# Kernel optimization log

Measured on AMD Instinct MI355X. Metric: run time of the kernel, lower is better.

Reference implementation:

```python
import jax, jax.numpy as jnp
import numpy as np

B, S, H = 1, 2048, 4096
NH = 32
HD = H // NH  # 128
HALF = HD // 2
BASE = 10000.0


def setup_inputs() -> dict:
    key = jax.random.key(0)
    k1, k2, k3 = jax.random.split(key, 3)
    hidden_states = jax.random.normal(k1, (B, S, H), dtype=jnp.float32)
    W_qkv = jax.random.normal(k2, (H, 3 * H), dtype=jnp.float32) * 0.02
    W_o = jax.random.normal(k3, (H, H), dtype=jnp.float32) * 0.02
    # causal additive mask [B,1,S,S]: 0 on/below diagonal, large negative above
    causal = jnp.triu(jnp.full((S, S), -1e9, dtype=jnp.float32), k=1)
    attention_mask = jnp.broadcast_to(causal[None, None], (B, 1, S, S))
    position_ids = jnp.broadcast_to(jnp.arange(S, dtype=jnp.int64)[None, :], (B, S))
    return {
        'hidden_states': hidden_states,
        'W_qkv': W_qkv,
        'W_o': W_o,
        'attention_mask': attention_mask,
        'position_ids': position_ids,
    }


def _rope(x, cos, sin):
    # x: [b,s,nh,hd]; cos/sin: [b,s,1,half]. Half-split rotation as in the Triton kernel.
    x1, x2 = x[..., :HALF], x[..., HALF:]
    return jnp.concatenate([x1 * cos - x2 * sin, x1 * sin + x2 * cos], axis=-1)


def reference(hidden_states, W_qkv, W_o, attention_mask, position_ids):
    b, s, h = hidden_states.shape
    # fused QKV projection (dequantized GPTQ matmul == dense matmul math)
    qkv = jnp.einsum('bsh,hk->bsk', hidden_states, W_qkv).reshape(b, s, 3, NH, HD)
    # RoPE angles: freq = exp(col * INV_BASE) * position_id, INV_BASE = -2 ln(base)/head_dim
    inv_base = -2.0 * np.log(BASE) / HD
    freqs = jnp.exp(jnp.arange(HALF, dtype=jnp.float32) * inv_base)  # [half]
    theta = position_ids.astype(jnp.float32)[:, :, None] * freqs      # [b,s,half]
    cos = jnp.cos(theta)[:, :, None, :]
    sin = jnp.sin(theta)[:, :, None, :]
    q = _rope(qkv[:, :, 0], cos, sin).transpose(0, 2, 1, 3)  # [b,nh,s,hd]
    k = _rope(qkv[:, :, 1], cos, sin).transpose(0, 2, 1, 3)
    v = qkv[:, :, 2].transpose(0, 2, 1, 3)
    scores = jnp.einsum('bhqd,bhkd->bhqk', q, k) / np.sqrt(HD).astype(np.float32)
    scores = scores + attention_mask
    scores = jnp.maximum(scores, jnp.finfo(scores.dtype).min)
    attn = jax.nn.softmax(scores.astype(jnp.float32), axis=-1).astype(q.dtype)
    out = jnp.einsum('bhqk,bhkd->bqhd', attn, v).reshape(b, s, h)
    return jnp.einsum('bsh,ho->bso', out, W_o)
```

## Files before the change

kernel.cpp:

```cpp
#include <hip/hip_runtime.h>

#define S_LEN 2048
#define HDIM 4096
#define NHEADS 32
#define HEAD_DIM 128
#define HALF_DIM 64
#define N_QKV 12288
#define QK_COLS 8192

typedef __attribute__((ext_vector_type(8))) short short8;
typedef __attribute__((ext_vector_type(4))) float f32x4;

typedef const __attribute__((address_space(1))) unsigned int gu32;
typedef __attribute__((address_space(3))) unsigned int lu32;

__device__ __forceinline__ void gload_lds16(const void* g, void* l) {
    __builtin_amdgcn_global_load_lds((gu32*)g, (lu32*)l, 16, 0, 0);
}

__device__ __forceinline__ unsigned short f2bf(float f) {
    unsigned int u = __float_as_uint(f);
    u += 0x7fff + ((u >> 16) & 1);
    return (unsigned short)(u >> 16);
}

__device__ __forceinline__ void xcd_map(int& bx, int& by) {
    int gx = gridDim.x;
    int lin = blockIdx.y * gx + blockIdx.x;
    int x = lin & 7, c = lin >> 3;
    int bxp = gx >> 3;
    bx = bxp * x + c % bxp;
    by = c / bxp;
}


__global__ __launch_bounds__(256) void cvt_hs_k(const float* __restrict__ in,
                                                unsigned short* __restrict__ out, int n4) {
    int i = blockIdx.x * 256 + threadIdx.x;
    if (i >= n4) return;
    float4 v = reinterpret_cast<const float4*>(in)[i];
    ushort4 o;
    o.x = f2bf(v.x); o.y = f2bf(v.y); o.z = f2bf(v.z); o.w = f2bf(v.w);
    reinterpret_cast<ushort4*>(out)[i] = o;
}

__device__ __forceinline__ int permute_col(int n) {
    if (n < QK_COLS) {
        int hd = n & 127;
        int base = n - hd;
        int e = hd & 63;
        int d2 = (e & 15) + 32 * (e >> 4) + ((hd >> 6) << 4);
        return base + d2;
    }
    return n;
}

template <bool PERM>
__global__ __launch_bounds__(256) void tconv_k(const float* __restrict__ in,
                                               unsigned short* __restrict__ out, int R, int C) {
    __shared__ float tile[64][65];
    int c0 = blockIdx.x * 64, r0 = blockIdx.y * 64;
    int tx = threadIdx.x & 63, ty = threadIdx.x >> 6;
#pragma unroll
    for (int i = 0; i < 16; ++i) {
        int r = ty + i * 4;
        tile[r][tx] = in[(size_t)(r0 + r) * C + c0 + tx];
    }
    __syncthreads();
#pragma unroll
    for (int i = 0; i < 16; ++i) {
        int c = ty + i * 4;
        int n = PERM ? permute_col(c0 + c) : (c0 + c);
        out[(size_t)n * R + r0 + tx] = f2bf(tile[tx][c]);
    }
}

__global__ __launch_bounds__(256) void rope_tab_k(const int* __restrict__ pos_raw,
                                                  float* __restrict__ ctab,
                                                  float* __restrict__ stab) {
    int i = blockIdx.x * 256 + threadIdx.x;
    int s = i >> 6, d = i & 63;
    bool is64 = (pos_raw[1] == 0 && pos_raw[2] == 1);
    int p = is64 ? pos_raw[2 * s] : pos_raw[s];
    const float INVB = -0.14391156831212787f;
    float freq = expf((float)d * INVB);
    float th = (float)p * freq;
    ctab[i] = cosf(th);
    stab[i] = sinf(th);
}


__device__ __forceinline__ void mainloop(const unsigned short* __restrict__ Ag,
                                         const unsigned short* __restrict__ Bg,
                                         int K, int m0, int n0,
                                         char* As, char* Bs,
                                         f32x4 (&acc)[4][4]) {
    const int tid = threadIdx.x;
    const int wid = tid >> 6, lane = tid & 63, l15 = lane & 15, l4 = lane >> 4;
    const int wm = wid >> 1, wn = wid & 1;
    const int NT = K >> 6;

    size_t abase[4], bbase[4];
    int off[4];
#pragma unroll
    for (int i = 0; i < 4; ++i) {
        int p = (i * 256 + tid) << 4;
        int q = p ^ (((p >> 7) & 7) << 4);
        abase[i] = (size_t)(m0 + (q >> 7)) * K + ((q & 127) >> 1);
        bbase[i] = (size_t)(n0 + (q >> 7)) * K + ((q & 127) >> 1);
        off[i] = p;
    }

    for (int t = 0; t < NT; ++t) {
        int k0 = t << 6;
#pragma unroll
        for (int i = 0; i < 4; ++i) gload_lds16(Ag + abase[i] + k0, As + off[i]);
#pragma unroll
        for (int i = 0; i < 4; ++i) gload_lds16(Bg + bbase[i] + k0, Bs + off[i]);
        asm volatile("s_waitcnt vmcnt(0)" ::: "memory");
        __builtin_amdgcn_s_barrier();

        short8 a[4][2], b[4][2];
#pragma unroll
        for (int am = 0; am < 4; ++am)
#pragma unroll
            for (int ks = 0; ks < 2; ++ks) {
                int lin = ((wm * 64 + am * 16 + l15) << 7) + ks * 64 + l4 * 16;
                a[am][ks] = *(const short8*)(As + (lin ^ (((lin >> 7) & 7) << 4)));
            }
#pragma unroll
        for (int bn = 0; bn < 4; ++bn)
#pragma unroll
            for (int ks = 0; ks < 2; ++ks) {
                int lin = ((wn * 64 + bn * 16 + l15) << 7) + ks * 64 + l4 * 16;
                b[bn][ks] = *(const short8*)(Bs + (lin ^ (((lin >> 7) & 7) << 4)));
            }
#pragma unroll
        for (int ks = 0; ks < 2; ++ks)
#pragma unroll
            for (int am = 0; am < 4; ++am)
#pragma unroll
                for (int bn = 0; bn < 4; ++bn)
                    acc[am][bn] = __builtin_amdgcn_mfma_f32_16x16x32_bf16(a[am][ks], b[bn][ks], acc[am][bn], 0, 0, 0);

        __builtin_amdgcn_s_barrier();
    }
}

__global__ __launch_bounds__(256, 3) void gemm1_k(const unsigned short* __restrict__ A,
                                                  const unsigned short* __restrict__ Bt,
                                                  const float* __restrict__ ctab,
                                                  const float* __restrict__ stab,
                                                  unsigned short* __restrict__ qb,
                                                  unsigned short* __restrict__ kb,
                                                  unsigned short* __restrict__ vt) {
    __shared__ __attribute__((aligned(16))) char As[16384];
    __shared__ __attribute__((aligned(16))) char Bs[16384];

    int bx, by;
    xcd_map(bx, by);
    int m0 = by * 128, n0 = bx * 128;

    f32x4 acc[4][4];
#pragma unroll
    for (int i = 0; i < 4; ++i)
#pragma unroll
        for (int j = 0; j < 4; ++j) acc[i][j] = (f32x4){0.f, 0.f, 0.f, 0.f};

    mainloop(A, Bt, HDIM, m0, n0, As, Bs, acc);

    int tid = threadIdx.x, wid = tid >> 6, lane = tid & 63, l15 = lane & 15, l4 = lane >> 4;
    int wm = wid >> 1, wn = wid & 1;
    int which = n0 >> 12;
    int head = (n0 & 4095) >> 7;
    if (which < 2) {
        unsigned short* dst = which ? kb : qb;
#pragma unroll
        for (int am = 0; am < 4; ++am)
#pragma unroll
            for (int j = 0; j < 4; ++j) {
                int s = m0 + wm * 64 + am * 16 + l4 * 4 + j;
#pragma unroll
                for (int p = 0; p < 2; ++p) {
                    float x1 = acc[am][2 * p][j], x2 = acc[am][2 * p + 1][j];
                    int e = l15 + 16 * (2 * wn + p);
                    float cs = ctab[s * 64 + e], sn = stab[s * 64 + e];
                    dst[((size_t)head * S_LEN + s) * HEAD_DIM + e] = f2bf(x1 * cs - x2 * sn);
                    dst[((size_t)head * S_LEN + s) * HEAD_DIM + e + 64] = f2bf(x1 * sn + x2 * cs);
                }
            }
    } else {
#pragma unroll
        for (int am = 0; am < 4; ++am)
#pragma unroll
            for (int j = 0; j < 4; ++j) {
                int s = m0 + wm * 64 + am * 16 + l4 * 4 + j;
#pragma unroll
                for (int bn = 0; bn < 4; ++bn) {
                    int d = wn * 64 + bn * 16 + l15;
                    vt[((size_t)head * HEAD_DIM + d) * S_LEN + s] = f2bf(acc[am][bn][j]);
                }
            }
    }
}

__global__ __launch_bounds__(256, 3) void gemm2_k(const unsigned short* __restrict__ A,
                                                  const unsigned short* __restrict__ Bt,
                                                  float* __restrict__ out) {
    __shared__ __attribute__((aligned(16))) char As[16384];
    __shared__ __attribute__((aligned(16))) char Bs[16384];

    int bx, by;
    xcd_map(bx, by);
    int m0 = by * 128, n0 = bx * 128;

    f32x4 acc[4][4];
#pragma unroll
    for (int i = 0; i < 4; ++i)
#pragma unroll
        for (int j = 0; j < 4; ++j) acc[i][j] = (f32x4){0.f, 0.f, 0.f, 0.f};

    mainloop(A, Bt, HDIM, m0, n0, As, Bs, acc);

    int tid = threadIdx.x, wid = tid >> 6, lane = tid & 63, l15 = lane & 15, l4 = lane >> 4;
    int wm = wid >> 1, wn = wid & 1;
#pragma unroll
    for (int am = 0; am < 4; ++am)
#pragma unroll
        for (int j = 0; j < 4; ++j) {
            int s = m0 + wm * 64 + am * 16 + l4 * 4 + j;
#pragma unroll
            for (int bn = 0; bn < 4; ++bn)
                out[(size_t)s * HDIM + n0 + wn * 64 + bn * 16 + l15] = acc[am][bn][j];
        }
}

__global__ __launch_bounds__(256) void flash_k(const unsigned short* __restrict__ Q,
                                               const unsigned short* __restrict__ Kb,
                                               const unsigned short* __restrict__ Vt,
                                               unsigned short* __restrict__ Ctx) {
    __shared__ __attribute__((aligned(16))) char Ks[2][16384];
    __shared__ __attribute__((aligned(16))) char Vs[2][16384];
    __shared__ __attribute__((aligned(16))) char Ps[4][4096];
    int qbk = (int)gridDim.x - 1 - blockIdx.x;
    int h = blockIdx.y;
    int tid = threadIdx.x, w = tid >> 6, lane = tid & 63, l15 = lane & 15, l4 = lane >> 4;
    int qrow0 = qbk * 128 + w * 32;

    const unsigned short* Kg = Kb + (size_t)h * S_LEN * HEAD_DIM;
    const unsigned short* Vg = Vt + (size_t)h * HEAD_DIM * S_LEN;

    short8 qf[2][4];
#pragma unroll
    for (int mt = 0; mt < 2; ++mt) {
        int s = qrow0 + mt * 16 + l15;
#pragma unroll
        for (int ks = 0; ks < 4; ++ks)
            qf[mt][ks] = *(const short8*)(Q + ((size_t)h * S_LEN + s) * HEAD_DIM + ks * 32 + l4 * 8);
    }

    float m_run[2][4];
    f32x4 o[2][8];
    f32x4 lsum[2];
#pragma unroll
    for (int mt = 0; mt < 2; ++mt) {
#pragma unroll
        for (int j = 0; j < 4; ++j) m_run[mt][j] = -1e30f;
        lsum[mt] = (f32x4){0.f, 0.f, 0.f, 0.f};
#pragma unroll
        for (int dt = 0; dt < 8; ++dt) o[mt][dt] = (f32x4){0.f, 0.f, 0.f, 0.f};
    }

    int lofs[4];
    size_t kgofs[4], vgofs[4];
#pragma unroll
    for (int i = 0; i < 4; ++i) {
        int p = (i * 256 + tid) << 4;
        lofs[i] = p;
        int qk = p ^ (((p >> 8) & 7) << 4);
        kgofs[i] = (size_t)(qk >> 8) * HEAD_DIM + ((qk & 255) >> 1);
        int qv = p ^ (((p >> 7) & 7) << 4);
        vgofs[i] = (size_t)(qv >> 7) * S_LEN + ((qv & 127) >> 1);
    }

    auto stage = [&](int t) {
        char* Kd = Ks[t & 1];
        char* Vd = Vs[t & 1];
        size_t kvoff = (size_t)t * 64;
#pragma unroll
        for (int i = 0; i < 4; ++i) gload_lds16(Kg + kvoff * HEAD_DIM + kgofs[i], Kd + lofs[i]);
#pragma unroll
        for (int i = 0; i < 4; ++i) gload_lds16(Vg + kvoff + vgofs[i], Vd + lofs[i]);
    };

    const float scale = 0.08838834764831845f;
    const int NT = 2 * (qbk + 1);

    short8 onesv;
#pragma unroll
    for (int e = 0; e < 8; ++e) onesv[e] = (short)0x3F80;

    stage(0);

    for (int t = 0; t < NT; ++t) {
        int cur = t & 1;
        if (t + 1 < NT) {
            stage(t + 1);
            asm volatile("s_waitcnt vmcnt(8)" ::: "memory");
        } else {
            asm volatile("s_waitcnt vmcnt(0)" ::: "memory");
        }
        __builtin_amdgcn_sched_barrier(0);
        __builtin_amdgcn_s_barrier();
        __builtin_amdgcn_sched_barrier(0);

        f32x4 sc[2][4];
#pragma unroll
        for (int mt = 0; mt < 2; ++mt)
#pragma unroll
            for (int nt = 0; nt < 4; ++nt) sc[mt][nt] = (f32x4){0.f, 0.f, 0.f, 0.f};
#pragma unroll
        for (int ks = 0; ks < 4; ++ks) {
            short8 kfr[4];
#pragma unroll
            for (int nt = 0; nt < 4; ++nt) {
                int lin = ((nt * 16 + l15) << 8) + ks * 64 + l4 * 16;
                kfr[nt] = *(const short8*)(Ks[cur] + (lin ^ (((lin >> 8) & 7) << 4)));
            }
#pragma unroll
            for (int mt = 0; mt < 2; ++mt)
#pragma unroll
                for (int nt = 0; nt < 4; ++nt)
                    sc[mt][nt] = __builtin_amdgcn_mfma_f32_16x16x32_bf16(qf[mt][ks], kfr[nt], sc[mt][nt], 0, 0, 0);
        }

        float pmax[2][4];
        bool need = false;
#pragma unroll
        for (int mt = 0; mt < 2; ++mt)
#pragma unroll
            for (int j = 0; j < 4; ++j) {
                int srow = qrow0 + mt * 16 + l4 * 4 + j;
                int c = t * 64 + l15;
                float v0 = (c      <= srow) ? sc[mt][0][j] * scale : -1e30f;
                float v1 = (c + 16 <= srow) ? sc[mt][1][j] * scale : -1e30f;
                float v2 = (c + 32 <= srow) ? sc[mt][2][j] * scale : -1e30f;
                float v3 = (c + 48 <= srow) ? sc[mt][3][j] * scale : -1e30f;
                sc[mt][0][j] = v0; sc[mt][1][j] = v1; sc[mt][2][j] = v2; sc[mt][3][j] = v3;
                float mx = fmaxf(fmaxf(v0, v1), fmaxf(v2, v3));
                mx = fmaxf(mx, __shfl_xor(mx, 1));
                mx = fmaxf(mx, __shfl_xor(mx, 2));
                mx = fmaxf(mx, __shfl_xor(mx, 4));
                mx = fmaxf(mx, __shfl_xor(mx, 8));
                pmax[mt][j] = mx;
                need = need || (mx > m_run[mt][j] + 8.0f);
            }
        if (__any(need ? 1 : 0)) {
#pragma unroll
            for (int mt = 0; mt < 2; ++mt)
#pragma unroll
                for (int j = 0; j < 4; ++j) {
                    float mnew = fmaxf(m_run[mt][j], pmax[mt][j]);
                    float r = __expf(m_run[mt][j] - mnew);
                    m_run[mt][j] = mnew;
                    lsum[mt][j] *= r;
#pragma unroll
                    for (int dt = 0; dt < 8; ++dt) o[mt][dt][j] *= r;
                }
        }

#pragma unroll
        for (int mt = 0; mt < 2; ++mt)
#pragma unroll
            for (int j = 0; j < 4; ++j) {
                int prow = mt * 16 + l4 * 4 + j;
                int rb = prow << 7;
                int sw = (prow & 7) << 4;
#pragma unroll
                for (int nt = 0; nt < 4; ++nt) {
                    unsigned short pb = f2bf(__expf(sc[mt][nt][j] - m_run[mt][j]));
                    *(unsigned short*)(Ps[w] + ((rb + (l15 + nt * 16) * 2) ^ sw)) = pb;
                }
            }
        asm volatile("s_waitcnt lgkmcnt(0)" ::: "memory");
        __builtin_amdgcn_sched_barrier(0);

        short8 pf[2][2];
#pragma unroll
        for (int mt = 0; mt < 2; ++mt)
#pragma unroll
            for (int k2 = 0; k2 < 2; ++k2) {
                int lin = ((mt * 16 + l15) << 7) + k2 * 64 + l4 * 16;
                pf[mt][k2] = *(const short8*)(Ps[w] + (lin ^ (((lin >> 7) & 7) << 4)));
            }
#pragma unroll
        for (int k2 = 0; k2 < 2; ++k2)
#pragma unroll
            for (int mt = 0; mt < 2; ++mt)
                lsum[mt] = __builtin_amdgcn_mfma_f32_16x16x32_bf16(pf[mt][k2], onesv, lsum[mt], 0, 0, 0);
#pragma unroll
        for (int dt = 0; dt < 8; ++dt) {
#pragma unroll
            for (int k2 = 0; k2 < 2; ++k2) {
                int lin = ((dt * 16 + l15) << 7) + k2 * 64 + l4 * 16;
                short8 vf = *(const short8*)(Vs[cur] + (lin ^ (((lin >> 7) & 7) << 4)));
#pragma unroll
                for (int mt = 0; mt < 2; ++mt)
                    o[mt][dt] = __builtin_amdgcn_mfma_f32_16x16x32_bf16(pf[mt][k2], vf, o[mt][dt], 0, 0, 0);
            }
        }
        __builtin_amdgcn_sched_barrier(0);
        __builtin_amdgcn_s_barrier();
        __builtin_amdgcn_sched_barrier(0);
    }

#pragma unroll
    for (int mt = 0; mt < 2; ++mt)
#pragma unroll
        for (int j = 0; j < 4; ++j) {
            float inv = 1.0f / lsum[mt][j];
            int s = qrow0 + mt * 16 + l4 * 4 + j;
#pragma unroll
            for (int dt = 0; dt < 8; ++dt)
                Ctx[(size_t)s * HDIM + h * HEAD_DIM + dt * 16 + l15] = f2bf(o[mt][dt][j] * inv);
        }
}


extern "C" void kernel_launch(void* const* d_in, const int* in_sizes, int n_in,
                              void* d_out, int out_size, void* d_ws, size_t ws_size,
                              hipStream_t stream) {
    const float* hs = (const float*)d_in[0];
    const float* wqkv = (const float*)d_in[1];
    const float* wo = (const float*)d_in[2];
    const int* pos = (const int*)d_in[4];
    float* out = (float*)d_out;
    char* ws = (char*)d_ws;
    const size_t MB = 1024 * 1024;

    unsigned short* hs_b = (unsigned short*)(ws);
    unsigned short* wq_t = (unsigned short*)(ws + 16 * MB);
    unsigned short* wo_t = (unsigned short*)(ws + 112 * MB);
    unsigned short* qbuf = (unsigned short*)(ws + 144 * MB);
    unsigned short* kbuf = (unsigned short*)(ws + 160 * MB);
    unsigned short* vtb  = (unsigned short*)(ws + 176 * MB);
    unsigned short* ctx  = (unsigned short*)(ws + 192 * MB);
    float* ctab = (float*)(ws + 208 * MB);
    float* stab = (float*)(ws + 209 * MB);

    cvt_hs_k<<<(S_LEN * HDIM / 4 + 255) / 256, 256, 0, stream>>>(hs, hs_b, S_LEN * HDIM / 4);
    tconv_k<true><<<dim3(N_QKV / 64, HDIM / 64), 256, 0, stream>>>(wqkv, wq_t, HDIM, N_QKV);
    tconv_k<false><<<dim3(HDIM / 64, HDIM / 64), 256, 0, stream>>>(wo, wo_t, HDIM, HDIM);
    rope_tab_k<<<(S_LEN * 64) / 256, 256, 0, stream>>>(pos, ctab, stab);
    gemm1_k<<<dim3(N_QKV / 128, S_LEN / 128), 256, 0, stream>>>(hs_b, wq_t, ctab, stab, qbuf, kbuf, vtb);
    flash_k<<<dim3(S_LEN / 128, NHEADS), 256, 0, stream>>>(qbuf, kbuf, vtb, ctx);
    gemm2_k<<<dim3(HDIM / 128, S_LEN / 128), 256, 0, stream>>>(ctx, wo_t, out);
}
```

Before: 591.3 us.

## Split causal flash attention across KV chunks and merge partials in a reduce kernel

Each query block's key/value range is split into chunks of up to 512 keys. Query blocks that see more of the causal range now get more splits, giving 40 work items per head instead of 16. Each work item writes unnormalized fp32 outputs plus its running max and sum. A new reduce kernel combines these with log-sum-exp weights and writes the bf16 context. The aim is to fix the causal load imbalance and give longer-row blocks more parallelism, at the cost of extra fp32 partial traffic, an extra launch, and reuse of the weight-transpose workspace region.

```diff
diff --git a/kernel.cpp b/kernel.cpp
--- a/kernel.cpp
+++ b/kernel.cpp
@@ -238,14 +238,25 @@
 __global__ __launch_bounds__(256) void flash_k(const unsigned short* __restrict__ Q,
                                                const unsigned short* __restrict__ Kb,
                                                const unsigned short* __restrict__ Vt,
-                                               unsigned short* __restrict__ Ctx) {
+                                               float* __restrict__ O_parts,
+                                               float* __restrict__ ml) {
     __shared__ __attribute__((aligned(16))) char Ks[2][16384];
     __shared__ __attribute__((aligned(16))) char Vs[2][16384];
     __shared__ __attribute__((aligned(16))) char Ps[4][4096];
-    int qbk = (int)gridDim.x - 1 - blockIdx.x;
     int h = blockIdx.y;
+    int bx2 = 39 - (int)blockIdx.x;
+    int qblk, spl;
+    if (bx2 < 4)       { qblk = bx2;                 spl = 0; }
+    else if (bx2 < 12) { qblk = 4 + ((bx2 - 4) >> 1);  spl = (bx2 - 4) & 1; }
+    else if (bx2 < 24) { int u = bx2 - 12; int q3 = u / 3; qblk = 8 + q3; spl = u - 3 * q3; }
+    else               { qblk = 12 + ((bx2 - 24) >> 2); spl = (bx2 - 24) & 3; }
+    int pidx = h * 40 + bx2;
+    int kv_start = spl << 9;
+    int kv_end = min((qblk + 1) << 7, (spl + 1) << 9);
+    int NT = (kv_end - kv_start) >> 6;
+
     int tid = threadIdx.x, w = tid >> 6, lane = tid & 63, l15 = lane & 15, l4 = lane >> 4;
-    int qrow0 = qbk * 128 + w * 32;
+    int qrow0 = qblk * 128 + w * 32;
 
     const unsigned short* Kg = Kb + (size_t)h * S_LEN * HEAD_DIM;
     const unsigned short* Vg = Vt + (size_t)h * HEAD_DIM * S_LEN;
@@ -286,7 +297,7 @@
     auto stage = [&](int t) {
         char* Kd = Ks[t & 1];
         char* Vd = Vs[t & 1];
-        size_t kvoff = (size_t)t * 64;
+        size_t kvoff = (size_t)(kv_start + t * 64);
 #pragma unroll
         for (int i = 0; i < 4; ++i) gload_lds16(Kg + kvoff * HEAD_DIM + kgofs[i], Kd + lofs[i]);
 #pragma unroll
@@ -294,7 +305,6 @@
     };
 
     const float scale = 0.08838834764831845f;
-    const int NT = 2 * (qbk + 1);
 
     short8 onesv;
 #pragma unroll
@@ -341,7 +351,7 @@
 #pragma unroll
             for (int j = 0; j < 4; ++j) {
                 int srow = qrow0 + mt * 16 + l4 * 4 + j;
-                int c = t * 64 + l15;
+                int c = kv_start + t * 64 + l15;
                 float v0 = (c      <= srow) ? sc[mt][0][j] * scale : -1e30f;
                 float v1 = (c + 16 <= srow) ? sc[mt][1][j] * scale : -1e30f;
                 float v2 = (c + 32 <= srow) ? sc[mt][2][j] * scale : -1e30f;
@@ -414,16 +424,57 @@
         __builtin_amdgcn_sched_barrier(0);
     }
 
+    float* Op = O_parts + (size_t)pidx * 16384;
 #pragma unroll
     for (int mt = 0; mt < 2; ++mt)
 #pragma unroll
         for (int j = 0; j < 4; ++j) {
-            float inv = 1.0f / lsum[mt][j];
-            int s = qrow0 + mt * 16 + l4 * 4 + j;
+            int rloc = w * 32 + mt * 16 + l4 * 4 + j;
 #pragma unroll
             for (int dt = 0; dt < 8; ++dt)
-                Ctx[(size_t)s * HDIM + h * HEAD_DIM + dt * 16 + l15] = f2bf(o[mt][dt][j] * inv);
-        }
+                Op[rloc * 128 + dt * 16 + l15] = o[mt][dt][j];
+            if (l15 == 0) {
+                ml[(size_t)pidx * 256 + rloc] = m_run[mt][j];
+                ml[(size_t)pidx * 256 + 128 + rloc] = lsum[mt][j];
+            }
+        }
+}
+
+__global__ __launch_bounds__(256) void reduce_k(const float* __restrict__ Op,
+                                                const float* __restrict__ ml,
+                                                unsigned short* __restrict__ ctx) {
+    int qblk = blockIdx.x, h = blockIdx.y;
+    int ns = (qblk >> 2) + 1;
+    int st;
+    if (qblk < 4) st = qblk;
+    else if (qblk < 8) st = 4 + 2 * (qblk - 4);
+    else if (qblk < 12) st = 12 + 3 * (qblk - 8);
+    else st = 24 + 4 * (qblk - 12);
+    int p0 = h * 40 + st;
+#pragma unroll
+    for (int it = 0; it < 16; ++it) {
+        int idx = it * 256 + threadIdx.x;
+        int row = idx >> 5, dq = idx & 31;
+        float mstar = -1e30f;
+        for (int s = 0; s < ns; ++s)
+            mstar = fmaxf(mstar, ml[(size_t)(p0 + s) * 256 + row]);
+        f32x4 acc = (f32x4){0.f, 0.f, 0.f, 0.f};
+        float lt = 0.f;
+        for (int s = 0; s < ns; ++s) {
+            float wgt = __expf(ml[(size_t)(p0 + s) * 256 + row] - mstar);
+            lt += wgt * ml[(size_t)(p0 + s) * 256 + 128 + row];
+            f32x4 ov = *(const f32x4*)(Op + (size_t)(p0 + s) * 16384 + row * 128 + dq * 4);
+            acc += ov * wgt;
+        }
+        float inv = 1.0f / lt;
+        int grow = qblk * 128 + row;
+        ushort4 o4;
+        o4.x = f2bf(acc[0] * inv);
+        o4.y = f2bf(acc[1] * inv);
+        o4.z = f2bf(acc[2] * inv);
+        o4.w = f2bf(acc[3] * inv);
+        *(ushort4*)(ctx + (size_t)grow * HDIM + h * 128 + dq * 4) = o4;
+    }
 }
 
 
@@ -447,12 +498,15 @@
     unsigned short* ctx  = (unsigned short*)(ws + 192 * MB);
     float* ctab = (float*)(ws + 208 * MB);
     float* stab = (float*)(ws + 209 * MB);
+    float* O_parts = (float*)(ws + 16 * MB);
+    float* ml_buf  = (float*)(ws + 96 * MB);
 
     cvt_hs_k<<<(S_LEN * HDIM / 4 + 255) / 256, 256, 0, stream>>>(hs, hs_b, S_LEN * HDIM / 4);
     tconv_k<true><<<dim3(N_QKV / 64, HDIM / 64), 256, 0, stream>>>(wqkv, wq_t, HDIM, N_QKV);
     tconv_k<false><<<dim3(HDIM / 64, HDIM / 64), 256, 0, stream>>>(wo, wo_t, HDIM, HDIM);
     rope_tab_k<<<(S_LEN * 64) / 256, 256, 0, stream>>>(pos, ctab, stab);
     gemm1_k<<<dim3(N_QKV / 128, S_LEN / 128), 256, 0, stream>>>(hs_b, wq_t, ctab, stab, qbuf, kbuf, vtb);
-    flash_k<<<dim3(S_LEN / 128, NHEADS), 256, 0, stream>>>(qbuf, kbuf, vtb, ctx);
+    flash_k<<<dim3(40, NHEADS), 256, 0, stream>>>(qbuf, kbuf, vtb, O_parts, ml_buf);
+    reduce_k<<<dim3(S_LEN / 128, NHEADS), 256, 0, stream>>>(O_parts, ml_buf, ctx);
     gemm2_k<<<dim3(HDIM / 128, S_LEN / 128), 256, 0, stream>>>(ctx, wo_t, out);
 }
```

Result: faster. 541.1 us (-8.5%).
